# Optimization experiments

Measured on AMD Instinct MI355X. Metric: run time of the kernel, lower is better.

Reference implementation:

```python
import jax, jax.numpy as jnp
import numpy as np

B, N, DIM = 4, 1024, 768
HEADS, DIM_HEAD = 12, 64
INNER = HEADS * DIM_HEAD  # 768
SCALE = DIM ** -0.5


def setup_inputs() -> dict:
    key = jax.random.key(0)
    ks = jax.random.split(key, 5)
    return {
        "x": jax.random.normal(ks[0], (B, N, DIM), dtype=jnp.float32),
        "pos_embedding": jax.random.normal(ks[1], (B, N, DIM), dtype=jnp.float32),
        "w_qkv": jax.random.normal(ks[2], (DIM, 3 * INNER), dtype=jnp.float32) * (DIM ** -0.5),
        "w_qk_pos": jax.random.normal(ks[3], (DIM, 2 * INNER), dtype=jnp.float32) * (DIM ** -0.5),
        "w_out": jax.random.normal(ks[4], (INNER, DIM), dtype=jnp.float32) * (INNER ** -0.5),
        "b_out": jnp.zeros((DIM,), dtype=jnp.float32),
    }


def _split_heads(t):
    # [b, n, h*d] -> [b, h, n, d]
    b, n, _ = t.shape
    return t.reshape(b, n, HEADS, DIM_HEAD).transpose(0, 2, 1, 3)


def reference(x, pos_embedding, w_qkv, w_qk_pos, w_out, b_out):
    qkv = x @ w_qkv  # [b, n, 3*inner]
    q, k, v = (_split_heads(t) for t in jnp.split(qkv, 3, axis=-1))
    qk_pos = pos_embedding @ w_qk_pos  # [b, n, 2*inner]
    q_pos, k_pos = (_split_heads(t) for t in jnp.split(qk_pos, 2, axis=-1))

    dots = jnp.einsum('bhid,bhjd->bhij', q, k) * SCALE
    dots_pos = jnp.einsum('bhid,bhjd->bhij', q_pos, k_pos) * SCALE
    dots = (dots + dots_pos) * 0.5  # averaged content+positional scores

    attn = jax.nn.softmax(dots, axis=-1)
    out = jnp.einsum('bhij,bhjd->bhid', attn, v)
    out = out.transpose(0, 2, 1, 3).reshape(x.shape[0], x.shape[1], INNER)
    return out @ w_out + b_out
```

## Files before the change

kernel.cpp:

```cpp
#include <hip/hip_runtime.h>
#include <cstdint>
#include <cstddef>

typedef __bf16 bf16;
typedef __bf16 bf16x8 __attribute__((ext_vector_type(8)));
typedef float  f32x4  __attribute__((ext_vector_type(4)));

#define MFMA(a, b, c) __builtin_amdgcn_mfma_f32_16x16x32_bf16((a), (b), (c), 0, 0, 0)

typedef __attribute__((address_space(3))) unsigned int  lds_u32;
typedef __attribute__((address_space(1))) unsigned int glob_u32;


__global__ void k_cvt2(const float* __restrict__ x, const float* __restrict__ pos,
                       bf16* __restrict__ xb, bf16* __restrict__ posb) {
    int i = blockIdx.x * 256 + threadIdx.x;
    const float* in = x; bf16* out = xb;
    if (i >= 786432) { i -= 786432; in = pos; out = posb; }
    float4 v = reinterpret_cast<const float4*>(in)[i];
    bf16 o0 = (bf16)v.x, o1 = (bf16)v.y, o2 = (bf16)v.z, o3 = (bf16)v.w;
    typedef __bf16 bf16x4v __attribute__((ext_vector_type(4)));
    bf16x4v o; o[0] = o0; o[1] = o1; o[2] = o2; o[3] = o3;
    reinterpret_cast<bf16x4v*>(out)[i] = o;
}

__global__ void k_tr(const float* __restrict__ w_qkv, const float* __restrict__ w_qk_pos,
                     const float* __restrict__ w_out,
                     bf16* __restrict__ wqkvT, bf16* __restrict__ wqkposT,
                     bf16* __restrict__ woutT) {
    __shared__ float t[32][33];
    int bx = blockIdx.x;
    const float* in; bf16* out; int N;
    if (bx < 72)       { in = w_qkv;    out = wqkvT;   N = 2304; }
    else if (bx < 120) { in = w_qk_pos; out = wqkposT; N = 1536; bx -= 72; }
    else               { in = w_out;    out = woutT;   N = 768;  bx -= 120; }
    const int n0 = bx * 32, k0 = blockIdx.y * 32;
    const int tx = threadIdx.x & 31, ty = threadIdx.x >> 5;
#pragma unroll
    for (int r = 0; r < 32; r += 8)
        t[ty + r][tx] = in[(size_t)(k0 + ty + r) * N + n0 + tx];
    __syncthreads();
#pragma unroll
    for (int r = 0; r < 32; r += 8)
        out[(size_t)(n0 + ty + r) * 768 + k0 + tx] = (bf16)t[tx][ty + r];
}

__launch_bounds__(256, 2)
__global__ void k_gemm12(const bf16* __restrict__ xb, const bf16* __restrict__ posb,
                         const bf16* __restrict__ wqkvT, const bf16* __restrict__ wqkposT,
                         bf16* __restrict__ qcat, bf16* __restrict__ kcat,
                         bf16* __restrict__ vT) {
    __shared__ bf16 lA[128][40];
    __shared__ bf16 lB[128][40];

    const int tid  = threadIdx.x;
    const int lane = tid & 63, wave = tid >> 6;
    const int quad = lane >> 4, col = lane & 15;
    const int wm = (wave >> 1) * 64, wn = (wave & 1) * 64;

    int bx = blockIdx.x, mode, nBase;
    const bf16 *A, *BT;
    if (bx < 18) { mode = 0; A = xb;   BT = wqkvT;   nBase = bx * 128; }
    else         { mode = 1; A = posb; BT = wqkposT; nBase = (bx - 18) * 128; }
    const int mBase = blockIdx.y * 128;

    const int r0 = tid >> 2, c0 = (tid & 3) * 8;
    const bf16* Ap = A  + (size_t)mBase * 768;
    const bf16* Bp = BT + (size_t)nBase * 768;

    uint4 a0 = *(const uint4*)(Ap + (size_t)r0 * 768 + c0);
    uint4 a1 = *(const uint4*)(Ap + (size_t)(r0 + 64) * 768 + c0);
    uint4 b0 = *(const uint4*)(Bp + (size_t)r0 * 768 + c0);
    uint4 b1 = *(const uint4*)(Bp + (size_t)(r0 + 64) * 768 + c0);

    f32x4 acc[4][4];
#pragma unroll
    for (int mi = 0; mi < 4; ++mi)
#pragma unroll
        for (int ni = 0; ni < 4; ++ni) acc[mi][ni] = f32x4{0.f, 0.f, 0.f, 0.f};

    for (int k0 = 0; k0 < 768; k0 += 32) {
        *(uint4*)&lA[r0][c0]      = a0;
        *(uint4*)&lA[r0 + 64][c0] = a1;
        *(uint4*)&lB[r0][c0]      = b0;
        *(uint4*)&lB[r0 + 64][c0] = b1;
        __syncthreads();
        if (k0 < 736) {
            const int kn = k0 + 32 + c0;
            a0 = *(const uint4*)(Ap + (size_t)r0 * 768 + kn);
            a1 = *(const uint4*)(Ap + (size_t)(r0 + 64) * 768 + kn);
            b0 = *(const uint4*)(Bp + (size_t)r0 * 768 + kn);
            b1 = *(const uint4*)(Bp + (size_t)(r0 + 64) * 768 + kn);
        }
        bf16x8 af[4], bfg[4];
#pragma unroll
        for (int mi = 0; mi < 4; ++mi) af[mi]  = *(const bf16x8*)&lA[wm + mi * 16 + col][quad * 8];
#pragma unroll
        for (int ni = 0; ni < 4; ++ni) bfg[ni] = *(const bf16x8*)&lB[wn + ni * 16 + col][quad * 8];
#pragma unroll
        for (int mi = 0; mi < 4; ++mi)
#pragma unroll
            for (int ni = 0; ni < 4; ++ni)
                acc[mi][ni] = MFMA(af[mi], bfg[ni], acc[mi][ni]);
        __syncthreads();
    }

#pragma unroll
    for (int mi = 0; mi < 4; ++mi)
#pragma unroll
        for (int ni = 0; ni < 4; ++ni)
#pragma unroll
            for (int r = 0; r < 4; ++r) {
                int m = mBase + wm + mi * 16 + quad * 4 + r;
                int n = nBase + wn + ni * 16 + col;
                float v = acc[mi][ni][r];
                int which = n / 768, rr = n - which * 768;
                int hh = rr >> 6, dd = rr & 63;
                int b = m >> 10, srow = m & 1023;
                size_t hb = (size_t)(b * 12 + hh);
                if (mode == 0) {
                    if (which == 0)      qcat[(hb * 1024 + srow) * 128 + dd] = (bf16)v;
                    else if (which == 1) kcat[(hb * 1024 + srow) * 128 + dd] = (bf16)v;
                    else                 vT[(hb * 64 + dd) * 1024 + srow]    = (bf16)v;
                } else {
                    if (which == 0)      qcat[(hb * 1024 + srow) * 128 + 64 + dd] = (bf16)v;
                    else                 kcat[(hb * 1024 + srow) * 128 + 64 + dd] = (bf16)v;
                }
            }
}

__launch_bounds__(256, 3)
__global__ void k_attn(const bf16* __restrict__ qcat, const bf16* __restrict__ kcat,
                       const bf16* __restrict__ vT, bf16* __restrict__ attn_out) {
    __shared__ bf16 lK[2][64][128];
    __shared__ bf16 lV[2][64][64];
    __shared__ bf16 lP[4][16][40];

    const int tid  = threadIdx.x;
    const int lane = tid & 63, wave = tid >> 6;
    const int quad = lane >> 4, col = lane & 15;
    const int sw   = col & 7;
    const int qt = blockIdx.x, h = blockIdx.y, b = blockIdx.z;
    const size_t hrow = (size_t)(b * 12 + h) * 1024;
    const bf16* Kb = kcat + hrow * 128;
    const bf16* Vb = vT + (size_t)(b * 12 + h) * 64 * 1024;

    const int kidx = wave * 256 + lane;
    const int vidx = wave * 128 + lane;

#define STAGE_K(buf, kv0)                                                      \
    _Pragma("unroll")                                                          \
    for (int j = 0; j < 4; ++j) {                                              \
        int idx = kidx + j * 64;                                               \
        int row = idx >> 4, c = idx & 15, csrc = c ^ (row & 7);                \
        __builtin_amdgcn_global_load_lds(                                      \
            (const glob_u32*)(Kb + (size_t)((kv0) + row) * 128 + csrc * 8),    \
            (lds_u32*)(&lK[buf][0][0] + (wave * 4 + j) * 512), 16, 0, 0);      \
    }
#define STAGE_V(buf, kv0)                                                      \
    _Pragma("unroll")                                                          \
    for (int j = 0; j < 2; ++j) {                                              \
        int idx = vidx + j * 64;                                               \
        int row = idx >> 3, c = idx & 7, csrc = c ^ (row & 7);                 \
        __builtin_amdgcn_global_load_lds(                                      \
            (const glob_u32*)(Vb + (size_t)row * 1024 + (kv0) + csrc * 8),     \
            (lds_u32*)(&lV[buf][0][0] + (wave * 2 + j) * 512), 16, 0, 0);      \
    }

    bf16x8 qf[4];
    {
        const bf16* qrow = qcat + (hrow + qt * 64 + wave * 16 + col) * 128;
#pragma unroll
        for (int f = 0; f < 4; ++f) qf[f] = *(const bf16x8*)(qrow + f * 32 + quad * 8);
    }

    f32x4 o[4];
#pragma unroll
    for (int t = 0; t < 4; ++t) o[t] = f32x4{0.f, 0.f, 0.f, 0.f};
    float lsum[4] = {0.f, 0.f, 0.f, 0.f};
    const float c2 = 0.018042195912f * 1.44269504089f;

    STAGE_K(0, 0)
    STAGE_V(0, 0)

    for (int it = 0; it < 16; ++it) {
        const int cur = it & 1, nxt = cur ^ 1;
        __syncthreads();
        if (it < 15) {
            const int kv1 = (it + 1) * 64;
            STAGE_K(nxt, kv1)
            STAGE_V(nxt, kv1)
        }

        f32x4 s[4];
#pragma unroll
        for (int t = 0; t < 4; ++t) s[t] = f32x4{0.f, 0.f, 0.f, 0.f};
#pragma unroll
        for (int t = 0; t < 4; ++t)
#pragma unroll
            for (int f = 0; f < 4; ++f) {
                bf16x8 kf = *(const bf16x8*)&lK[cur][t * 16 + col][((f * 4 + quad) ^ sw) * 8];
                s[t] = MFMA(qf[f], kf, s[t]);
            }

#pragma unroll
        for (int t = 0; t < 4; ++t)
#pragma unroll
            for (int r = 0; r < 4; ++r) s[t][r] = exp2f(s[t][r] * c2);
#pragma unroll
        for (int r = 0; r < 4; ++r)
            lsum[r] += (s[0][r] + s[1][r]) + (s[2][r] + s[3][r]);

#pragma unroll
        for (int half = 0; half < 2; ++half) {
#pragma unroll
            for (int r = 0; r < 4; ++r)
#pragma unroll
                for (int t2 = 0; t2 < 2; ++t2)
                    lP[wave][quad * 4 + r][t2 * 16 + col] = (bf16)s[half * 2 + t2][r];
            bf16x8 pf = *(const bf16x8*)&lP[wave][col][quad * 8];
#pragma unroll
            for (int t = 0; t < 4; ++t) {
                bf16x8 vf = *(const bf16x8*)&lV[cur][t * 16 + col][((half * 4 + quad) ^ sw) * 8];
                o[t] = MFMA(pf, vf, o[t]);
            }
        }
    }

#pragma unroll
    for (int r = 0; r < 4; ++r) {
        float l = lsum[r];
#pragma unroll
        for (int off = 1; off < 16; off <<= 1) l += __shfl_xor(l, off, 64);
        float inv = 1.f / l;
        int row = qt * 64 + wave * 16 + quad * 4 + r;
#pragma unroll
        for (int t = 0; t < 4; ++t)
            attn_out[((size_t)b * 1024 + row) * 768 + h * 64 + t * 16 + col] =
                (bf16)(o[t][r] * inv);
    }
#undef STAGE_K
#undef STAGE_V
}

__launch_bounds__(256, 2)
__global__ void k_gemm_out(const bf16* __restrict__ aout, const bf16* __restrict__ woutT,
                           const float* __restrict__ bias, float* __restrict__ out) {
    __shared__ bf16 lA[128][40];
    __shared__ bf16 lB[64][40];

    const int tid  = threadIdx.x;
    const int lane = tid & 63, wave = tid >> 6;
    const int quad = lane >> 4, col = lane & 15;
    const int wm = (wave >> 1) * 64, wn = (wave & 1) * 32;
    const int mBase = blockIdx.y * 128, nBase = blockIdx.x * 64;

    const int r0 = tid >> 2, c0 = (tid & 3) * 8;
    const bf16* Ap = aout  + (size_t)mBase * 768;
    const bf16* Bp = woutT + (size_t)nBase * 768;

    uint4 a0 = *(const uint4*)(Ap + (size_t)r0 * 768 + c0);
    uint4 a1 = *(const uint4*)(Ap + (size_t)(r0 + 64) * 768 + c0);
    uint4 b0 = *(const uint4*)(Bp + (size_t)r0 * 768 + c0);

    f32x4 acc[4][2];
#pragma unroll
    for (int mi = 0; mi < 4; ++mi)
#pragma unroll
        for (int ni = 0; ni < 2; ++ni) acc[mi][ni] = f32x4{0.f, 0.f, 0.f, 0.f};

    for (int k0 = 0; k0 < 768; k0 += 32) {
        *(uint4*)&lA[r0][c0]      = a0;
        *(uint4*)&lA[r0 + 64][c0] = a1;
        *(uint4*)&lB[r0][c0]      = b0;
        __syncthreads();
        if (k0 < 736) {
            const int kn = k0 + 32 + c0;
            a0 = *(const uint4*)(Ap + (size_t)r0 * 768 + kn);
            a1 = *(const uint4*)(Ap + (size_t)(r0 + 64) * 768 + kn);
            b0 = *(const uint4*)(Bp + (size_t)r0 * 768 + kn);
        }
        bf16x8 af[4], bfg[2];
#pragma unroll
        for (int mi = 0; mi < 4; ++mi) af[mi]  = *(const bf16x8*)&lA[wm + mi * 16 + col][quad * 8];
#pragma unroll
        for (int ni = 0; ni < 2; ++ni) bfg[ni] = *(const bf16x8*)&lB[wn + ni * 16 + col][quad * 8];
#pragma unroll
        for (int mi = 0; mi < 4; ++mi)
#pragma unroll
            for (int ni = 0; ni < 2; ++ni)
                acc[mi][ni] = MFMA(af[mi], bfg[ni], acc[mi][ni]);
        __syncthreads();
    }

#pragma unroll
    for (int mi = 0; mi < 4; ++mi)
#pragma unroll
        for (int ni = 0; ni < 2; ++ni)
#pragma unroll
            for (int r = 0; r < 4; ++r) {
                int m = mBase + wm + mi * 16 + quad * 4 + r;
                int n = nBase + wn + ni * 16 + col;
                out[(size_t)m * 768 + n] = acc[mi][ni][r] + bias[n];
            }
}

extern "C" void kernel_launch(void* const* d_in, const int* in_sizes, int n_in,
                              void* d_out, int out_size, void* d_ws, size_t ws_size,
                              hipStream_t stream) {
    const float* x        = (const float*)d_in[0];
    const float* pos      = (const float*)d_in[1];
    const float* w_qkv    = (const float*)d_in[2];
    const float* w_qk_pos = (const float*)d_in[3];
    const float* w_out    = (const float*)d_in[4];
    const float* b_out    = (const float*)d_in[5];
    float* out = (float*)d_out;

    char* ws = (char*)d_ws;
    bf16* xb      = (bf16*)(ws);
    bf16* posb    = (bf16*)(ws + 6291456);
    bf16* wqkvT   = (bf16*)(ws + 12582912);
    bf16* wqkposT = (bf16*)(ws + 16121856);
    bf16* woutT   = (bf16*)(ws + 18481152);
    bf16* qcat    = (bf16*)(ws + 19660800);
    bf16* kcat    = (bf16*)(ws + 32243712);
    bf16* vT      = (bf16*)(ws + 44826624);
    bf16* aout    = (bf16*)(ws + 51118080);

    k_cvt2<<<6144, 256, 0, stream>>>(x, pos, xb, posb);
    k_tr<<<dim3(144, 24), 256, 0, stream>>>(w_qkv, w_qk_pos, w_out, wqkvT, wqkposT, woutT);
    k_gemm12<<<dim3(30, 32), 256, 0, stream>>>(xb, posb, wqkvT, wqkposT, qcat, kcat, vT);
    k_attn<<<dim3(16, 12, 4), 256, 0, stream>>>(qcat, kcat, vT, aout);
    k_gemm_out<<<dim3(12, 32), 256, 0, stream>>>(aout, woutT, b_out, out);
}
```

Measured before the change: 210.5 us.

## Double-buffer GEMM tiles via direct global-to-LDS loads with XOR swizzle

```diff
diff --git a/kernel.cpp b/kernel.cpp
--- a/kernel.cpp
+++ b/kernel.cpp
@@ -4,6 +4,7 @@
 
 typedef __bf16 bf16;
 typedef __bf16 bf16x8 __attribute__((ext_vector_type(8)));
+typedef __bf16 bf16x4v __attribute__((ext_vector_type(4)));
 typedef float  f32x4  __attribute__((ext_vector_type(4)));
 
 #define MFMA(a, b, c) __builtin_amdgcn_mfma_f32_16x16x32_bf16((a), (b), (c), 0, 0, 0)
@@ -18,9 +19,7 @@
     const float* in = x; bf16* out = xb;
     if (i >= 786432) { i -= 786432; in = pos; out = posb; }
     float4 v = reinterpret_cast<const float4*>(in)[i];
-    bf16 o0 = (bf16)v.x, o1 = (bf16)v.y, o2 = (bf16)v.z, o3 = (bf16)v.w;
-    typedef __bf16 bf16x4v __attribute__((ext_vector_type(4)));
-    bf16x4v o; o[0] = o0; o[1] = o1; o[2] = o2; o[3] = o3;
+    bf16x4v o; o[0] = (bf16)v.x; o[1] = (bf16)v.y; o[2] = (bf16)v.z; o[3] = (bf16)v.w;
     reinterpret_cast<bf16x4v*>(out)[i] = o;
 }
 
@@ -45,17 +44,18 @@
         out[(size_t)(n0 + ty + r) * 768 + k0 + tx] = (bf16)t[tx][ty + r];
 }
 
-__launch_bounds__(256, 2)
+__launch_bounds__(256, 3)
 __global__ void k_gemm12(const bf16* __restrict__ xb, const bf16* __restrict__ posb,
                          const bf16* __restrict__ wqkvT, const bf16* __restrict__ wqkposT,
                          bf16* __restrict__ qcat, bf16* __restrict__ kcat,
                          bf16* __restrict__ vT) {
-    __shared__ bf16 lA[128][40];
-    __shared__ bf16 lB[128][40];
+    __shared__ bf16 lA[2][128][32];
+    __shared__ bf16 lB[2][128][32];
 
     const int tid  = threadIdx.x;
     const int lane = tid & 63, wave = tid >> 6;
     const int quad = lane >> 4, col = lane & 15;
+    const int sw2  = (col >> 1) & 3;
     const int wm = (wave >> 1) * 64, wn = (wave & 1) * 64;
 
     int bx = blockIdx.x, mode, nBase;
@@ -64,14 +64,21 @@
     else         { mode = 1; A = posb; BT = wqkposT; nBase = (bx - 18) * 128; }
     const int mBase = blockIdx.y * 128;
 
-    const int r0 = tid >> 2, c0 = (tid & 3) * 8;
     const bf16* Ap = A  + (size_t)mBase * 768;
     const bf16* Bp = BT + (size_t)nBase * 768;
 
-    uint4 a0 = *(const uint4*)(Ap + (size_t)r0 * 768 + c0);
-    uint4 a1 = *(const uint4*)(Ap + (size_t)(r0 + 64) * 768 + c0);
-    uint4 b0 = *(const uint4*)(Bp + (size_t)r0 * 768 + c0);
-    uint4 b1 = *(const uint4*)(Bp + (size_t)(r0 + 64) * 768 + c0);
+#define STAGE12(buf, k0)                                                        \
+    _Pragma("unroll")                                                           \
+    for (int j = 0; j < 2; ++j) {                                               \
+        int idx = (wave * 2 + j) * 64 + lane;                                   \
+        int row = idx >> 2, c = (idx & 3) ^ ((row >> 1) & 3);                   \
+        __builtin_amdgcn_global_load_lds(                                       \
+            (const glob_u32*)(Ap + (size_t)row * 768 + (k0) + c * 8),           \
+            (lds_u32*)((char*)&lA[buf][0][0] + (wave * 2 + j) * 1024), 16, 0, 0);\
+        __builtin_amdgcn_global_load_lds(                                       \
+            (const glob_u32*)(Bp + (size_t)row * 768 + (k0) + c * 8),           \
+            (lds_u32*)((char*)&lB[buf][0][0] + (wave * 2 + j) * 1024), 16, 0, 0);\
+    }
 
     f32x4 acc[4][4];
 #pragma unroll
@@ -79,54 +86,56 @@
 #pragma unroll
         for (int ni = 0; ni < 4; ++ni) acc[mi][ni] = f32x4{0.f, 0.f, 0.f, 0.f};
 
-    for (int k0 = 0; k0 < 768; k0 += 32) {
-        *(uint4*)&lA[r0][c0]      = a0;
-        *(uint4*)&lA[r0 + 64][c0] = a1;
-        *(uint4*)&lB[r0][c0]      = b0;
-        *(uint4*)&lB[r0 + 64][c0] = b1;
+    STAGE12(0, 0)
+    for (int it = 0; it < 24; ++it) {
+        const int cur = it & 1, nxt = cur ^ 1;
         __syncthreads();
-        if (k0 < 736) {
-            const int kn = k0 + 32 + c0;
-            a0 = *(const uint4*)(Ap + (size_t)r0 * 768 + kn);
-            a1 = *(const uint4*)(Ap + (size_t)(r0 + 64) * 768 + kn);
-            b0 = *(const uint4*)(Bp + (size_t)r0 * 768 + kn);
-            b1 = *(const uint4*)(Bp + (size_t)(r0 + 64) * 768 + kn);
-        }
+        if (it < 23) STAGE12(nxt, (it + 1) * 32)
+
         bf16x8 af[4], bfg[4];
 #pragma unroll
-        for (int mi = 0; mi < 4; ++mi) af[mi]  = *(const bf16x8*)&lA[wm + mi * 16 + col][quad * 8];
-#pragma unroll
-        for (int ni = 0; ni < 4; ++ni) bfg[ni] = *(const bf16x8*)&lB[wn + ni * 16 + col][quad * 8];
+        for (int mi = 0; mi < 4; ++mi)
+            af[mi]  = *(const bf16x8*)&lA[cur][wm + mi * 16 + col][(quad ^ sw2) * 8];
+#pragma unroll
+        for (int ni = 0; ni < 4; ++ni)
+            bfg[ni] = *(const bf16x8*)&lB[cur][wn + ni * 16 + col][(quad ^ sw2) * 8];
 #pragma unroll
         for (int mi = 0; mi < 4; ++mi)
 #pragma unroll
             for (int ni = 0; ni < 4; ++ni)
                 acc[mi][ni] = MFMA(af[mi], bfg[ni], acc[mi][ni]);
-        __syncthreads();
-    }
-
-#pragma unroll
-    for (int mi = 0; mi < 4; ++mi)
-#pragma unroll
-        for (int ni = 0; ni < 4; ++ni)
-#pragma unroll
-            for (int r = 0; r < 4; ++r) {
-                int m = mBase + wm + mi * 16 + quad * 4 + r;
-                int n = nBase + wn + ni * 16 + col;
-                float v = acc[mi][ni][r];
-                int which = n / 768, rr = n - which * 768;
-                int hh = rr >> 6, dd = rr & 63;
-                int b = m >> 10, srow = m & 1023;
-                size_t hb = (size_t)(b * 12 + hh);
-                if (mode == 0) {
-                    if (which == 0)      qcat[(hb * 1024 + srow) * 128 + dd] = (bf16)v;
-                    else if (which == 1) kcat[(hb * 1024 + srow) * 128 + dd] = (bf16)v;
-                    else                 vT[(hb * 64 + dd) * 1024 + srow]    = (bf16)v;
-                } else {
-                    if (which == 0)      qcat[(hb * 1024 + srow) * 128 + 64 + dd] = (bf16)v;
-                    else                 kcat[(hb * 1024 + srow) * 128 + 64 + dd] = (bf16)v;
-                }
+    }
+#undef STAGE12
+
+    const int bb = mBase >> 10;
+    const int sr0 = (mBase & 1023) + wm + quad * 4;
+#pragma unroll
+    for (int ni = 0; ni < 4; ++ni) {
+        const int nb = nBase + wn + ni * 16;
+        const int which = (mode == 0) ? (nb >= 1536 ? 2 : (nb >= 768 ? 1 : 0))
+                                      : (nb >= 768 ? 1 : 0);
+        const int rem = nb - which * 768;
+        const int hh = rem >> 6, dd0 = rem & 63;
+        const size_t hb = (size_t)(bb * 12 + hh);
+        if (mode == 0 && which == 2) {
+            bf16* dstv = vT + (hb * 64 + dd0 + col) * 1024 + sr0;
+#pragma unroll
+            for (int mi = 0; mi < 4; ++mi) {
+                bf16x4v pk;
+#pragma unroll
+                for (int r = 0; r < 4; ++r) pk[r] = (bf16)acc[mi][ni][r];
+                *(bf16x4v*)(dstv + mi * 16) = pk;
             }
+        } else {
+            bf16* dstq = (which == 0 ? qcat : kcat)
+                       + (hb * 1024 + sr0) * 128 + (mode == 1 ? 64 : 0) + dd0 + col;
+#pragma unroll
+            for (int mi = 0; mi < 4; ++mi)
+#pragma unroll
+                for (int r = 0; r < 4; ++r)
+                    dstq[(size_t)(mi * 16 + r) * 128] = (bf16)acc[mi][ni][r];
+        }
+    }
 }
 
 __launch_bounds__(256, 3)
@@ -243,25 +252,38 @@
 #undef STAGE_V
 }
 
-__launch_bounds__(256, 2)
+__launch_bounds__(256, 3)
 __global__ void k_gemm_out(const bf16* __restrict__ aout, const bf16* __restrict__ woutT,
                            const float* __restrict__ bias, float* __restrict__ out) {
-    __shared__ bf16 lA[128][40];
-    __shared__ bf16 lB[64][40];
+    __shared__ bf16 lA[2][128][32];
+    __shared__ bf16 lB[2][64][32];
 
     const int tid  = threadIdx.x;
     const int lane = tid & 63, wave = tid >> 6;
     const int quad = lane >> 4, col = lane & 15;
+    const int sw2  = (col >> 1) & 3;
     const int wm = (wave >> 1) * 64, wn = (wave & 1) * 32;
     const int mBase = blockIdx.y * 128, nBase = blockIdx.x * 64;
 
-    const int r0 = tid >> 2, c0 = (tid & 3) * 8;
     const bf16* Ap = aout  + (size_t)mBase * 768;
     const bf16* Bp = woutT + (size_t)nBase * 768;
 
-    uint4 a0 = *(const uint4*)(Ap + (size_t)r0 * 768 + c0);
-    uint4 a1 = *(const uint4*)(Ap + (size_t)(r0 + 64) * 768 + c0);
-    uint4 b0 = *(const uint4*)(Bp + (size_t)r0 * 768 + c0);
+#define STAGE_O(buf, k0)                                                        \
+    _Pragma("unroll")                                                           \
+    for (int j = 0; j < 2; ++j) {                                               \
+        int idx = (wave * 2 + j) * 64 + lane;                                   \
+        int row = idx >> 2, c = (idx & 3) ^ ((row >> 1) & 3);                   \
+        __builtin_amdgcn_global_load_lds(                                       \
+            (const glob_u32*)(Ap + (size_t)row * 768 + (k0) + c * 8),           \
+            (lds_u32*)((char*)&lA[buf][0][0] + (wave * 2 + j) * 1024), 16, 0, 0);\
+    }                                                                           \
+    {                                                                           \
+        int idx = wave * 64 + lane;                                             \
+        int row = idx >> 2, c = (idx & 3) ^ ((row >> 1) & 3);                   \
+        __builtin_amdgcn_global_load_lds(                                       \
+            (const glob_u32*)(Bp + (size_t)row * 768 + (k0) + c * 8),           \
+            (lds_u32*)((char*)&lB[buf][0][0] + wave * 1024), 16, 0, 0);         \
+    }
 
     f32x4 acc[4][2];
 #pragma unroll
@@ -269,29 +291,26 @@
 #pragma unroll
         for (int ni = 0; ni < 2; ++ni) acc[mi][ni] = f32x4{0.f, 0.f, 0.f, 0.f};
 
-    for (int k0 = 0; k0 < 768; k0 += 32) {
-        *(uint4*)&lA[r0][c0]      = a0;
-        *(uint4*)&lA[r0 + 64][c0] = a1;
-        *(uint4*)&lB[r0][c0]      = b0;
+    STAGE_O(0, 0)
+    for (int it = 0; it < 24; ++it) {
+        const int cur = it & 1, nxt = cur ^ 1;
         __syncthreads();
-        if (k0 < 736) {
-            const int kn = k0 + 32 + c0;
-            a0 = *(const uint4*)(Ap + (size_t)r0 * 768 + kn);
-            a1 = *(const uint4*)(Ap + (size_t)(r0 + 64) * 768 + kn);
-            b0 = *(const uint4*)(Bp + (size_t)r0 * 768 + kn);
-        }
+        if (it < 23) STAGE_O(nxt, (it + 1) * 32)
+
         bf16x8 af[4], bfg[2];
 #pragma unroll
-        for (int mi = 0; mi < 4; ++mi) af[mi]  = *(const bf16x8*)&lA[wm + mi * 16 + col][quad * 8];
-#pragma unroll
-        for (int ni = 0; ni < 2; ++ni) bfg[ni] = *(const bf16x8*)&lB[wn + ni * 16 + col][quad * 8];
+        for (int mi = 0; mi < 4; ++mi)
+            af[mi]  = *(const bf16x8*)&lA[cur][wm + mi * 16 + col][(quad ^ sw2) * 8];
+#pragma unroll
+        for (int ni = 0; ni < 2; ++ni)
+            bfg[ni] = *(const bf16x8*)&lB[cur][wn + ni * 16 + col][(quad ^ sw2) * 8];
 #pragma unroll
         for (int mi = 0; mi < 4; ++mi)
 #pragma unroll
             for (int ni = 0; ni < 2; ++ni)
                 acc[mi][ni] = MFMA(af[mi], bfg[ni], acc[mi][ni]);
-        __syncthreads();
-    }
+    }
+#undef STAGE_O
 
 #pragma unroll
     for (int mi = 0; mi < 4; ++mi)
```

After: 198.1 us. -5.9%, faster.
